# Performance work log

Hardware: AMD Instinct MI355X
Metric: run time of the kernel (lower is better)

The kernel has to match this reference:

```python
import jax, jax.numpy as jnp
import numpy as np

B, N, E, H = 8, 512, 128, 64


def setup_inputs() -> dict:
    key = jax.random.key(0)
    k1, k2, k3 = jax.random.split(key, 3)
    h_freq = jax.random.normal(k1, (B * N, E), dtype=jnp.float32)
    W = jax.random.normal(k2, (2 * E, H), dtype=jnp.float32) * 0.05  # Linear(2E -> H) weight, stored input-major
    b = jnp.zeros((H,), dtype=jnp.float32)
    att = jax.random.normal(k3, (H,), dtype=jnp.float32) * 0.1
    return {"h_freq": h_freq, "W": W, "b": b, "att": att, "batch": B, "n_nodes": N}


def reference(h_freq, W, b, att, batch, n_nodes):
    n = n_nodes
    bsz = h_freq.shape[0] // n
    h = h_freq.reshape(bsz, n, -1)  # [B, N, E]
    # Fused form of cat([hj, hk]) @ W: split W into the hj-half and hk-half.
    W1, W2 = W[: h.shape[-1]], W[h.shape[-1]:]
    pj = h @ W1  # [B, N, H]
    pk = h @ W2  # [B, N, H]
    u = jax.nn.leaky_relu(pj[:, :, None, :] + pk[:, None, :, :] + b, negative_slope=0.2)  # [B, N, N, H]
    e = jnp.einsum("bjkh,h->bjk", u, att)  # [B, N, N]
    alpha = jax.nn.softmax(e, axis=2)
    # dense_to_sparse with learn_sys=True: symmetrize, drop diagonal (eval mode: no dropout)
    dense = (alpha + jnp.swapaxes(alpha, -1, -2)) * 0.5
    mask = ~np.eye(n, dtype=bool)
    src, dst = np.nonzero(mask)  # static, length n*(n-1)
    src = jnp.asarray(src, dtype=jnp.int64)
    dst = jnp.asarray(dst, dtype=jnp.int64)
    single = jnp.stack([src, dst], axis=0)  # [2, M]
    offsets = (jnp.arange(bsz, dtype=jnp.int64) * n)
    edge_index = (single[:, None, :] + offsets[None, :, None]).reshape(2, -1)  # [2, B*M]
    edge_weights = dense[:, src, dst].reshape(-1)  # [B*M]
    return edge_index, edge_weights, alpha
```

## Files before the change

### kernel.cpp

```cpp
#include <hip/hip_runtime.h>
#include <hip/hip_bf16.h>

#define BB 8
#define NN 512
#define EE 128
#define HH 64
#define EP (NN * (NN - 1))
#define ECNT (BB * EP)
#define OFF_EI0 0
#define OFF_EI1 ECNT
#define OFF_EW  (2 * ECNT)
#define OFF_AL  (3 * ECNT)

__global__ __launch_bounds__(256) void k_proj(
        const float* __restrict__ h, const float* __restrict__ W,
        const float* __restrict__ bvec, const float* __restrict__ att,
        float* __restrict__ pj, float* __restrict__ pkT4f,
        float* __restrict__ cj, float* __restrict__ dk) {
    __shared__ float Wl[2 * EE * HH];
    const int tid = threadIdx.x;

    {
        float4* Wl4 = reinterpret_cast<float4*>(Wl);
        const float4* W4 = reinterpret_cast<const float4*>(W);
#pragma unroll
        for (int r = 0; r < 16; ++r) Wl4[r * 256 + tid] = W4[r * 256 + tid];
    }

    const int row0 = blockIdx.x * 8;
    const int c = tid & 63;
    const int w = tid >> 6;
    const float* hA = h + (size_t)(row0 + w) * EE;
    const float* hB = h + (size_t)(row0 + w + 4) * EE;
    __syncthreads();

    float aj0 = 0.f, ak0 = 0.f, aj1 = 0.f, ak1 = 0.f;
#pragma unroll
    for (int e = 0; e < EE; ++e) {
        const float w1 = Wl[e * HH + c];
        const float w2 = Wl[(EE + e) * HH + c];
        const float h0 = hA[e];
        const float h1 = hB[e];
        aj0 = fmaf(h0, w1, aj0);
        ak0 = fmaf(h0, w2, ak0);
        aj1 = fmaf(h1, w1, aj1);
        ak1 = fmaf(h1, w2, ak1);
    }
    const float bb = bvec[c];
    aj0 += bb; aj1 += bb;

    const float a6 = 0.6f * att[c];
    const int iA = row0 + w;
    const int iB = row0 + w + 4;
    pj[iA * HH + c] = aj0;
    pj[iB * HH + c] = aj1;
    {
        const int bA = iA >> 9, nA = iA & 511;
        const int bB = iB >> 9, nB = iB & 511;
        pkT4f[(((size_t)(bA * 16 + (c >> 2)) * NN + nA) << 2) + (c & 3)] = ak0;
        pkT4f[(((size_t)(bB * 16 + (c >> 2)) * NN + nB) << 2) + (c & 3)] = ak1;
    }
    float c0 = a6 * aj0, d0 = a6 * ak0, c1 = a6 * aj1, d1 = a6 * ak1;
#pragma unroll
    for (int off = 32; off >= 1; off >>= 1) {
        c0 += __shfl_xor(c0, off, 64);
        d0 += __shfl_xor(d0, off, 64);
        c1 += __shfl_xor(c1, off, 64);
        d1 += __shfl_xor(d1, off, 64);
    }
    if (c == 0) {
        cj[iA] = c0; dk[iA] = d0;
        cj[iB] = c1; dk[iB] = d1;
    }
}

__global__ __launch_bounds__(512, 2) void k_attn(
        const float* __restrict__ pj, const float4* __restrict__ pkT4,
        const float* __restrict__ att, const float* __restrict__ cj,
        const float* __restrict__ dk, float* __restrict__ alpha) {
    const int bid   = blockIdx.x;
    const int b     = bid >> 6;
    const int jbase = (bid & 63) * 8;
    const int tid   = threadIdx.x;
    const int lane  = tid & 63;
    const int wid   = tid >> 6;

    __shared__ float4 pj4[8][HH / 4];
    __shared__ float  e_s[8][NN];

    if (tid < 128) {
        const int j = tid >> 4, q = tid & 15;
        pj4[j][q] = reinterpret_cast<const float4*>(
            pj + ((size_t)b * NN + jbase + j) * HH)[q];
    }

    float4 pk4[16];
    const float4* pkb = pkT4 + (size_t)b * 16 * NN + tid;
#pragma unroll
    for (int q = 0; q < 16; ++q) pk4[q] = pkb[q * NN];
    const float dkv = dk[b * NN + tid];
    const float* cjb = cj + b * NN + jbase;

    __syncthreads();

    float acc[8];
#pragma unroll
    for (int j = 0; j < 8; ++j) acc[j] = 0.f;

#pragma unroll
    for (int q = 0; q < 16; ++q) {
        const float4 af = reinterpret_cast<const float4*>(att)[q];
        const float4 kv = pk4[q];
#pragma unroll
        for (int j = 0; j < 8; ++j) {
            const float4 pw = pj4[j][q];
            float s;
            s = pw.x + kv.x; acc[j] = fmaf(af.x, fabsf(s), acc[j]);
            s = pw.y + kv.y; acc[j] = fmaf(af.y, fabsf(s), acc[j]);
            s = pw.z + kv.z; acc[j] = fmaf(af.z, fabsf(s), acc[j]);
            s = pw.w + kv.w; acc[j] = fmaf(af.w, fabsf(s), acc[j]);
        }
    }

#pragma unroll
    for (int j = 0; j < 8; ++j)
        e_s[j][tid] = fmaf(0.4f, acc[j], cjb[j] + dkv);
    __syncthreads();

    {
        float v[8];
        float m = -1e30f;
#pragma unroll
        for (int i2 = 0; i2 < 8; ++i2) {
            v[i2] = e_s[wid][lane + 64 * i2];
            m = fmaxf(m, v[i2]);
        }
#pragma unroll
        for (int off = 32; off >= 1; off >>= 1) m = fmaxf(m, __shfl_xor(m, off, 64));
        float s = 0.f;
#pragma unroll
        for (int i2 = 0; i2 < 8; ++i2) { v[i2] = __expf(v[i2] - m); s += v[i2]; }
#pragma unroll
        for (int off = 32; off >= 1; off >>= 1) s += __shfl_xor(s, off, 64);
        const float inv = 1.0f / s;
        float* arow = alpha + ((size_t)b * NN + jbase + wid) * NN;
#pragma unroll
        for (int i2 = 0; i2 < 8; ++i2) arow[lane + 64 * i2] = v[i2] * inv;
    }
}

__global__ void k_edges(const float* __restrict__ alpha, float* __restrict__ out) {
    const int bid = blockIdx.x;
    const int b   = bid / 36;
    int rem = bid - b * 36;
    int jt = 0;
    while (rem >= 8 - jt) { rem -= 8 - jt; ++jt; }
    const int kt = jt + rem;

    const int jbase = jt * 64;
    const int kbase = kt * 64;
    const int tid   = threadIdx.x;
    const int c     = tid & 63;
    const int r0    = tid >> 6;

    __shared__ float t1[64][65];
    __shared__ float t2[64][65];

    const float* A = alpha + (size_t)b * NN * NN;
    const bool diag = (jt == kt);

#pragma unroll
    for (int i = 0; i < 16; ++i) {
        const int r = i * 4 + r0;
        t1[r][c] = A[(size_t)(jbase + r) * NN + kbase + c];
    }
    if (!diag) {
#pragma unroll
        for (int i = 0; i < 16; ++i) {
            const int r = i * 4 + r0;
            t2[r][c] = A[(size_t)(kbase + r) * NN + jbase + c];
        }
    }
    __syncthreads();

    const float fb = (float)(b * NN);

#pragma unroll
    for (int i = 0; i < 16; ++i) {
        const int jj = i * 4 + r0;
        const int j  = jbase + jj;
        const int k  = kbase + c;
        if (k == j) continue;
        const float a_kj = diag ? t1[c][jj] : t2[c][jj];
        const float wv = 0.5f * (t1[jj][c] + a_kj);
        const unsigned t   = (unsigned)k - ((k > j) ? 1u : 0u);
        const unsigned idx = (unsigned)b * EP + (unsigned)j * (NN - 1) + t;
        out[OFF_EI0 + idx] = fb + (float)j;
        out[OFF_EI1 + idx] = fb + (float)k;
        out[OFF_EW  + idx] = wv;
    }

    if (!diag) {
#pragma unroll
        for (int i = 0; i < 16; ++i) {
            const int kk = i * 4 + r0;
            const int j2 = kbase + kk;
            const int k2 = jbase + c;
            const float wv = 0.5f * (t2[kk][c] + t1[c][kk]);
            const unsigned t   = (unsigned)k2 - ((k2 > j2) ? 1u : 0u);
            const unsigned idx = (unsigned)b * EP + (unsigned)j2 * (NN - 1) + t;
            out[OFF_EI0 + idx] = fb + (float)j2;
            out[OFF_EI1 + idx] = fb + (float)k2;
            out[OFF_EW  + idx] = wv;
        }
    }
}

extern "C" void kernel_launch(void* const* d_in, const int* in_sizes, int n_in,
                              void* d_out, int out_size, void* d_ws, size_t ws_size,
                              hipStream_t stream) {
    const float* h    = (const float*)d_in[0];
    const float* W    = (const float*)d_in[1];
    const float* bvec = (const float*)d_in[2];
    const float* att  = (const float*)d_in[3];
    float* out = (float*)d_out;

    float* pj   = (float*)d_ws;
    float* pkT4 = pj + (size_t)BB * NN * HH;
    float* cj   = pkT4 + (size_t)BB * NN * HH;
    float* dk   = cj + BB * NN;

    float* alpha = out + OFF_AL;

    k_proj <<<BB * NN / 8, 256, 0, stream>>>(h, W, bvec, att, pj, pkT4, cj, dk);
    k_attn <<<BB * 64, 512, 0, stream>>>(pj, (const float4*)pkT4, att, cj, dk, alpha);
    k_edges<<<BB * 36, 256, 0, stream>>>(alpha, out);
}
```

Measured before the change: 40.89 us.

## Drop W LDS staging in projection, fold dk into attention, drop cj term

The projection kernel no longer copies the full 64KB W matrix into shared memory in every block. Each wave now computes 8 rows directly against W read from global/L2, and the kernel stops producing cj and dk. The attention kernel computes the dk term itself from the pk values it already loads. It drops the per-row cj term, which is constant along the softmax axis and cancels in the softmax. It also uses 256 threads that each handle two k columns, and reads pj directly from global memory instead of staging it in LDS. The trade-off is higher register pressure and likely lower occupancy in the attention kernel, in exchange for fewer kernel outputs and far less redundant W traffic.

```diff
diff --git a/kernel.cpp b/kernel.cpp
--- a/kernel.cpp
+++ b/kernel.cpp
@@ -12,72 +12,61 @@
 #define OFF_EW  (2 * ECNT)
 #define OFF_AL  (3 * ECNT)
 
-__global__ __launch_bounds__(256) void k_proj(
+__global__ __launch_bounds__(128) void k_proj(
         const float* __restrict__ h, const float* __restrict__ W,
-        const float* __restrict__ bvec, const float* __restrict__ att,
-        float* __restrict__ pj, float* __restrict__ pkT4f,
-        float* __restrict__ cj, float* __restrict__ dk) {
-    __shared__ float Wl[2 * EE * HH];
-    const int tid = threadIdx.x;
-
-    {
-        float4* Wl4 = reinterpret_cast<float4*>(Wl);
-        const float4* W4 = reinterpret_cast<const float4*>(W);
-#pragma unroll
-        for (int r = 0; r < 16; ++r) Wl4[r * 256 + tid] = W4[r * 256 + tid];
-    }
-
-    const int row0 = blockIdx.x * 8;
-    const int c = tid & 63;
-    const int w = tid >> 6;
-    const float* hA = h + (size_t)(row0 + w) * EE;
-    const float* hB = h + (size_t)(row0 + w + 4) * EE;
-    __syncthreads();
-
-    float aj0 = 0.f, ak0 = 0.f, aj1 = 0.f, ak1 = 0.f;
-#pragma unroll
+        const float* __restrict__ bvec,
+        float* __restrict__ pj, float* __restrict__ pkT4f) {
+    const int tid  = threadIdx.x;
+    const int c    = tid & 63;
+    const int w    = tid >> 6;
+    const int row0 = blockIdx.x * 16 + w * 8;
+
+    const float* h0 = h + (size_t)(row0 + 0) * EE;
+    const float* h1 = h + (size_t)(row0 + 1) * EE;
+    const float* h2 = h + (size_t)(row0 + 2) * EE;
+    const float* h3 = h + (size_t)(row0 + 3) * EE;
+    const float* h4 = h + (size_t)(row0 + 4) * EE;
+    const float* h5 = h + (size_t)(row0 + 5) * EE;
+    const float* h6 = h + (size_t)(row0 + 6) * EE;
+    const float* h7 = h + (size_t)(row0 + 7) * EE;
+
+    float aj0=0.f,aj1=0.f,aj2=0.f,aj3=0.f,aj4=0.f,aj5=0.f,aj6=0.f,aj7=0.f;
+    float ak0=0.f,ak1=0.f,ak2=0.f,ak3=0.f,ak4=0.f,ak5=0.f,ak6=0.f,ak7=0.f;
+
+#pragma unroll 8
     for (int e = 0; e < EE; ++e) {
-        const float w1 = Wl[e * HH + c];
-        const float w2 = Wl[(EE + e) * HH + c];
-        const float h0 = hA[e];
-        const float h1 = hB[e];
-        aj0 = fmaf(h0, w1, aj0);
-        ak0 = fmaf(h0, w2, ak0);
-        aj1 = fmaf(h1, w1, aj1);
-        ak1 = fmaf(h1, w2, ak1);
+        const float w1 = W[e * HH + c];
+        const float w2 = W[(EE + e) * HH + c];
+        aj0 = fmaf(h0[e], w1, aj0); ak0 = fmaf(h0[e], w2, ak0);
+        aj1 = fmaf(h1[e], w1, aj1); ak1 = fmaf(h1[e], w2, ak1);
+        aj2 = fmaf(h2[e], w1, aj2); ak2 = fmaf(h2[e], w2, ak2);
+        aj3 = fmaf(h3[e], w1, aj3); ak3 = fmaf(h3[e], w2, ak3);
+        aj4 = fmaf(h4[e], w1, aj4); ak4 = fmaf(h4[e], w2, ak4);
+        aj5 = fmaf(h5[e], w1, aj5); ak5 = fmaf(h5[e], w2, ak5);
+        aj6 = fmaf(h6[e], w1, aj6); ak6 = fmaf(h6[e], w2, ak6);
+        aj7 = fmaf(h7[e], w1, aj7); ak7 = fmaf(h7[e], w2, ak7);
     }
     const float bb = bvec[c];
-    aj0 += bb; aj1 += bb;
-
-    const float a6 = 0.6f * att[c];
-    const int iA = row0 + w;
-    const int iB = row0 + w + 4;
-    pj[iA * HH + c] = aj0;
-    pj[iB * HH + c] = aj1;
-    {
-        const int bA = iA >> 9, nA = iA & 511;
-        const int bB = iB >> 9, nB = iB & 511;
-        pkT4f[(((size_t)(bA * 16 + (c >> 2)) * NN + nA) << 2) + (c & 3)] = ak0;
-        pkT4f[(((size_t)(bB * 16 + (c >> 2)) * NN + nB) << 2) + (c & 3)] = ak1;
-    }
-    float c0 = a6 * aj0, d0 = a6 * ak0, c1 = a6 * aj1, d1 = a6 * ak1;
-#pragma unroll
-    for (int off = 32; off >= 1; off >>= 1) {
-        c0 += __shfl_xor(c0, off, 64);
-        d0 += __shfl_xor(d0, off, 64);
-        c1 += __shfl_xor(c1, off, 64);
-        d1 += __shfl_xor(d1, off, 64);
-    }
-    if (c == 0) {
-        cj[iA] = c0; dk[iA] = d0;
-        cj[iB] = c1; dk[iB] = d1;
-    }
-}
-
-__global__ __launch_bounds__(512, 2) void k_attn(
+
+#define PROJ_WRITE(r, ajr, akr) {                                              \
+        const int i  = row0 + (r);                                             \
+        pj[i * HH + c] = (ajr) + bb;                                           \
+        const int bI = i >> 9, n = i & 511;                                    \
+        pkT4f[((((size_t)(bI * 16 + (c >> 2))) * NN + n) << 2) + (c & 3)] = (akr); }
+    PROJ_WRITE(0, aj0, ak0)
+    PROJ_WRITE(1, aj1, ak1)
+    PROJ_WRITE(2, aj2, ak2)
+    PROJ_WRITE(3, aj3, ak3)
+    PROJ_WRITE(4, aj4, ak4)
+    PROJ_WRITE(5, aj5, ak5)
+    PROJ_WRITE(6, aj6, ak6)
+    PROJ_WRITE(7, aj7, ak7)
+#undef PROJ_WRITE
+}
+
+__global__ __launch_bounds__(256, 2) void k_attn(
         const float* __restrict__ pj, const float4* __restrict__ pkT4,
-        const float* __restrict__ att, const float* __restrict__ cj,
-        const float* __restrict__ dk, float* __restrict__ alpha) {
+        const float* __restrict__ att, float* __restrict__ alpha) {
     const int bid   = blockIdx.x;
     const int b     = bid >> 6;
     const int jbase = (bid & 63) * 8;
@@ -85,54 +74,71 @@
     const int lane  = tid & 63;
     const int wid   = tid >> 6;
 
-    __shared__ float4 pj4[8][HH / 4];
-    __shared__ float  e_s[8][NN];
-
-    if (tid < 128) {
-        const int j = tid >> 4, q = tid & 15;
-        pj4[j][q] = reinterpret_cast<const float4*>(
-            pj + ((size_t)b * NN + jbase + j) * HH)[q];
-    }
-
-    float4 pk4[16];
+    __shared__ float e_s[8][NN];
+
+    float4 pkA[16], pkB[16];
     const float4* pkb = pkT4 + (size_t)b * 16 * NN + tid;
 #pragma unroll
-    for (int q = 0; q < 16; ++q) pk4[q] = pkb[q * NN];
-    const float dkv = dk[b * NN + tid];
-    const float* cjb = cj + b * NN + jbase;
-
+    for (int q = 0; q < 16; ++q) {
+        pkA[q] = pkb[q * NN];
+        pkB[q] = pkb[q * NN + 256];
+    }
+
+    const float4* att4 = reinterpret_cast<const float4*>(att);
+
+    float dkA = 0.f, dkB = 0.f;
+#pragma unroll
+    for (int q = 0; q < 16; ++q) {
+        const float4 a = att4[q];
+        dkA = fmaf(a.x, pkA[q].x, dkA); dkA = fmaf(a.y, pkA[q].y, dkA);
+        dkA = fmaf(a.z, pkA[q].z, dkA); dkA = fmaf(a.w, pkA[q].w, dkA);
+        dkB = fmaf(a.x, pkB[q].x, dkB); dkB = fmaf(a.y, pkB[q].y, dkB);
+        dkB = fmaf(a.z, pkB[q].z, dkB); dkB = fmaf(a.w, pkB[q].w, dkB);
+    }
+    dkA *= 0.6f; dkB *= 0.6f;
+
+    const float4* pjb4 = reinterpret_cast<const float4*>(
+        pj + ((size_t)b * NN + jbase) * HH);
+
+    float accA[8], accB[8];
+#pragma unroll
+    for (int j = 0; j < 8; ++j) { accA[j] = 0.f; accB[j] = 0.f; }
+
+#pragma unroll
+    for (int q = 0; q < 16; ++q) {
+        const float4 af = att4[q];
+        const float4 kA = pkA[q];
+        const float4 kB = pkB[q];
+#pragma unroll
+        for (int j = 0; j < 8; ++j) {
+            const float4 pw = pjb4[j * 16 + q];
+            float s;
+            s = pw.x + kA.x; accA[j] = fmaf(af.x, fabsf(s), accA[j]);
+            s = pw.y + kA.y; accA[j] = fmaf(af.y, fabsf(s), accA[j]);
+            s = pw.z + kA.z; accA[j] = fmaf(af.z, fabsf(s), accA[j]);
+            s = pw.w + kA.w; accA[j] = fmaf(af.w, fabsf(s), accA[j]);
+            s = pw.x + kB.x; accB[j] = fmaf(af.x, fabsf(s), accB[j]);
+            s = pw.y + kB.y; accB[j] = fmaf(af.y, fabsf(s), accB[j]);
+            s = pw.z + kB.z; accB[j] = fmaf(af.z, fabsf(s), accB[j]);
+            s = pw.w + kB.w; accB[j] = fmaf(af.w, fabsf(s), accB[j]);
+        }
+    }
+
+#pragma unroll
+    for (int j = 0; j < 8; ++j) {
+        e_s[j][tid]       = fmaf(0.4f, accA[j], dkA);
+        e_s[j][tid + 256] = fmaf(0.4f, accB[j], dkB);
+    }
     __syncthreads();
 
-    float acc[8];
-#pragma unroll
-    for (int j = 0; j < 8; ++j) acc[j] = 0.f;
-
-#pragma unroll
-    for (int q = 0; q < 16; ++q) {
-        const float4 af = reinterpret_cast<const float4*>(att)[q];
-        const float4 kv = pk4[q];
-#pragma unroll
-        for (int j = 0; j < 8; ++j) {
-            const float4 pw = pj4[j][q];
-            float s;
-            s = pw.x + kv.x; acc[j] = fmaf(af.x, fabsf(s), acc[j]);
-            s = pw.y + kv.y; acc[j] = fmaf(af.y, fabsf(s), acc[j]);
-            s = pw.z + kv.z; acc[j] = fmaf(af.z, fabsf(s), acc[j]);
-            s = pw.w + kv.w; acc[j] = fmaf(af.w, fabsf(s), acc[j]);
-        }
-    }
-
-#pragma unroll
-    for (int j = 0; j < 8; ++j)
-        e_s[j][tid] = fmaf(0.4f, acc[j], cjb[j] + dkv);
-    __syncthreads();
-
-    {
+#pragma unroll
+    for (int rr = 0; rr < 2; ++rr) {
+        const int j = wid + rr * 4;
         float v[8];
         float m = -1e30f;
 #pragma unroll
         for (int i2 = 0; i2 < 8; ++i2) {
-            v[i2] = e_s[wid][lane + 64 * i2];
+            v[i2] = e_s[j][lane + 64 * i2];
             m = fmaxf(m, v[i2]);
         }
 #pragma unroll
@@ -143,7 +149,7 @@
 #pragma unroll
         for (int off = 32; off >= 1; off >>= 1) s += __shfl_xor(s, off, 64);
         const float inv = 1.0f / s;
-        float* arow = alpha + ((size_t)b * NN + jbase + wid) * NN;
+        float* arow = alpha + ((size_t)b * NN + jbase + j) * NN;
 #pragma unroll
         for (int i2 = 0; i2 < 8; ++i2) arow[lane + 64 * i2] = v[i2] * inv;
     }
@@ -227,12 +233,10 @@
 
     float* pj   = (float*)d_ws;
     float* pkT4 = pj + (size_t)BB * NN * HH;
-    float* cj   = pkT4 + (size_t)BB * NN * HH;
-    float* dk   = cj + BB * NN;
 
     float* alpha = out + OFF_AL;
 
-    k_proj <<<BB * NN / 8, 256, 0, stream>>>(h, W, bvec, att, pj, pkT4, cj, dk);
-    k_attn <<<BB * 64, 512, 0, stream>>>(pj, (const float4*)pkT4, att, cj, dk, alpha);
+    k_proj <<<BB * NN / 16, 128, 0, stream>>>(h, W, bvec, pj, pkT4);
+    k_attn <<<BB * 64, 256, 0, stream>>>(pj, (const float4*)pkT4, att, alpha);
     k_edges<<<BB * 36, 256, 0, stream>>>(alpha, out);
 }
```

Result: slower. 54.86 us (+34.2%).

## Drop softmax-invariant row term, recompute dk in-kernel, load pj via scalar loads

Applied to the files above, without the earlier changes.

The per-row constant cj is removed because it cancels in the softmax over k, and the per-column term dk is now computed inside the attention kernel from the pk values already held in registers. This lets the projection kernel skip its shuffle reductions and extra writes. The pj rows are fetched with inline s_load_dwordx16 into scalar registers instead of being staged through LDS, so the VALU can read them as uniform operands. In exchange there is an explicit s_waitcnt per row that serializes the scalar loads, the inline asm is fragile, and the min-blocks launch bound is dropped.

```diff
diff --git a/kernel.cpp b/kernel.cpp
--- a/kernel.cpp
+++ b/kernel.cpp
@@ -12,11 +12,12 @@
 #define OFF_EW  (2 * ECNT)
 #define OFF_AL  (3 * ECNT)
 
+typedef float f16v __attribute__((ext_vector_type(16)));
+
 __global__ __launch_bounds__(256) void k_proj(
         const float* __restrict__ h, const float* __restrict__ W,
-        const float* __restrict__ bvec, const float* __restrict__ att,
-        float* __restrict__ pj, float* __restrict__ pkT4f,
-        float* __restrict__ cj, float* __restrict__ dk) {
+        const float* __restrict__ bvec,
+        float* __restrict__ pj, float* __restrict__ pkT4f) {
     __shared__ float Wl[2 * EE * HH];
     const int tid = threadIdx.x;
 
@@ -49,7 +50,6 @@
     const float bb = bvec[c];
     aj0 += bb; aj1 += bb;
 
-    const float a6 = 0.6f * att[c];
     const int iA = row0 + w;
     const int iB = row0 + w + 4;
     pj[iA * HH + c] = aj0;
@@ -60,24 +60,11 @@
         pkT4f[(((size_t)(bA * 16 + (c >> 2)) * NN + nA) << 2) + (c & 3)] = ak0;
         pkT4f[(((size_t)(bB * 16 + (c >> 2)) * NN + nB) << 2) + (c & 3)] = ak1;
     }
-    float c0 = a6 * aj0, d0 = a6 * ak0, c1 = a6 * aj1, d1 = a6 * ak1;
-#pragma unroll
-    for (int off = 32; off >= 1; off >>= 1) {
-        c0 += __shfl_xor(c0, off, 64);
-        d0 += __shfl_xor(d0, off, 64);
-        c1 += __shfl_xor(c1, off, 64);
-        d1 += __shfl_xor(d1, off, 64);
-    }
-    if (c == 0) {
-        cj[iA] = c0; dk[iA] = d0;
-        cj[iB] = c1; dk[iB] = d1;
-    }
-}
-
-__global__ __launch_bounds__(512, 2) void k_attn(
+}
+
+__global__ __launch_bounds__(512) void k_attn(
         const float* __restrict__ pj, const float4* __restrict__ pkT4,
-        const float* __restrict__ att, const float* __restrict__ cj,
-        const float* __restrict__ dk, float* __restrict__ alpha) {
+        const float* __restrict__ att, float* __restrict__ alpha) {
     const int bid   = blockIdx.x;
     const int b     = bid >> 6;
     const int jbase = (bid & 63) * 8;
@@ -85,46 +72,56 @@
     const int lane  = tid & 63;
     const int wid   = tid >> 6;
 
-    __shared__ float4 pj4[8][HH / 4];
-    __shared__ float  e_s[8][NN];
-
-    if (tid < 128) {
-        const int j = tid >> 4, q = tid & 15;
-        pj4[j][q] = reinterpret_cast<const float4*>(
-            pj + ((size_t)b * NN + jbase + j) * HH)[q];
-    }
+    __shared__ float e_s[8][NN];
 
     float4 pk4[16];
     const float4* pkb = pkT4 + (size_t)b * 16 * NN + tid;
 #pragma unroll
     for (int q = 0; q < 16; ++q) pk4[q] = pkb[q * NN];
-    const float dkv = dk[b * NN + tid];
-    const float* cjb = cj + b * NN + jbase;
-
-    __syncthreads();
-
-    float acc[8];
-#pragma unroll
-    for (int j = 0; j < 8; ++j) acc[j] = 0.f;
-
+
+    float4 att4[16];
+#pragma unroll
+    for (int q = 0; q < 16; ++q) att4[q] = reinterpret_cast<const float4*>(att)[q];
+
+    float dkv = 0.f;
 #pragma unroll
     for (int q = 0; q < 16; ++q) {
-        const float4 af = reinterpret_cast<const float4*>(att)[q];
-        const float4 kv = pk4[q];
-#pragma unroll
-        for (int j = 0; j < 8; ++j) {
-            const float4 pw = pj4[j][q];
+        dkv = fmaf(att4[q].x, pk4[q].x, dkv);
+        dkv = fmaf(att4[q].y, pk4[q].y, dkv);
+        dkv = fmaf(att4[q].z, pk4[q].z, dkv);
+        dkv = fmaf(att4[q].w, pk4[q].w, dkv);
+    }
+    dkv *= 0.6f;
+
+    const float* pjrow0 = pj + ((size_t)b * NN + jbase) * HH;
+
+#pragma unroll
+    for (int jj = 0; jj < 8; ++jj) {
+        const float* rp = pjrow0 + jj * HH;
+        f16v r0, r1, r2, r3;
+        asm volatile(
+            "s_load_dwordx16 %0, %4, 0x0\n\t"
+            "s_load_dwordx16 %1, %4, 0x40\n\t"
+            "s_load_dwordx16 %2, %4, 0x80\n\t"
+            "s_load_dwordx16 %3, %4, 0xC0\n\t"
+            "s_waitcnt lgkmcnt(0)"
+            : "=&s"(r0), "=&s"(r1), "=&s"(r2), "=&s"(r3)
+            : "s"(rp));
+#define PJH(h) ((h) < 16 ? r0[(h) & 15] : (h) < 32 ? r1[(h) & 15] : (h) < 48 ? r2[(h) & 15] : r3[(h) & 15])
+        float acc = 0.f;
+#pragma unroll
+        for (int q = 0; q < 16; ++q) {
+            const float4 kv = pk4[q];
+            const float4 af = att4[q];
             float s;
-            s = pw.x + kv.x; acc[j] = fmaf(af.x, fabsf(s), acc[j]);
-            s = pw.y + kv.y; acc[j] = fmaf(af.y, fabsf(s), acc[j]);
-            s = pw.z + kv.z; acc[j] = fmaf(af.z, fabsf(s), acc[j]);
-            s = pw.w + kv.w; acc[j] = fmaf(af.w, fabsf(s), acc[j]);
-        }
-    }
-
-#pragma unroll
-    for (int j = 0; j < 8; ++j)
-        e_s[j][tid] = fmaf(0.4f, acc[j], cjb[j] + dkv);
+            s = PJH(4 * q + 0) + kv.x; acc = fmaf(af.x, fabsf(s), acc);
+            s = PJH(4 * q + 1) + kv.y; acc = fmaf(af.y, fabsf(s), acc);
+            s = PJH(4 * q + 2) + kv.z; acc = fmaf(af.z, fabsf(s), acc);
+            s = PJH(4 * q + 3) + kv.w; acc = fmaf(af.w, fabsf(s), acc);
+        }
+#undef PJH
+        e_s[jj][tid] = fmaf(0.4f, acc, dkv);
+    }
     __syncthreads();
 
     {
@@ -227,12 +224,10 @@
 
     float* pj   = (float*)d_ws;
     float* pkT4 = pj + (size_t)BB * NN * HH;
-    float* cj   = pkT4 + (size_t)BB * NN * HH;
-    float* dk   = cj + BB * NN;
 
     float* alpha = out + OFF_AL;
 
-    k_proj <<<BB * NN / 8, 256, 0, stream>>>(h, W, bvec, att, pj, pkT4, cj, dk);
-    k_attn <<<BB * 64, 512, 0, stream>>>(pj, (const float4*)pkT4, att, cj, dk, alpha);
+    k_proj <<<BB * NN / 8, 256, 0, stream>>>(h, W, bvec, pj, pkT4);
+    k_attn <<<BB * 64, 512, 0, stream>>>(pj, (const float4*)pkT4, att, alpha);
     k_edges<<<BB * 36, 256, 0, stream>>>(alpha, out);
 }
```

After: 43.75 us. 7.0% more time.
